# Performance work log

Hardware: AMD Instinct MI355X
Metric: run time of the kernel (lower is better)

Reference implementation:

```python
import jax, jax.numpy as jnp
import numpy as np
from jax import lax

B, C_IN, L = 16, 4, 300000
KERNEL, ANCHOR_N = 11, 16
LEAK = 1e-4
EPS = 1e-12  # torch F.normalize eps


def setup_inputs() -> dict:
    key = jax.random.key(0)
    k1, k2, k3 = jax.random.split(key, 3)
    data = jax.random.normal(k1, (B, C_IN, L), dtype=jnp.float32)
    # Conv1d weights, PyTorch default init scale ~ U(-s, s), s = 1/sqrt(fan_in)
    s = 1.0 / np.sqrt(C_IN * KERNEL)
    W = jax.random.uniform(k2, (ANCHOR_N, C_IN, KERNEL), dtype=jnp.float32, minval=-s, maxval=s)
    b = jax.random.uniform(k3, (ANCHOR_N,), dtype=jnp.float32, minval=-s, maxval=s)
    return {"data": data, "W": W, "b": b, "anchor_index": 3}


def reference(data, W, b, anchor_index):
    # Conv1d(4 -> anchor_n, valid padding) + LeakyReLU(0.0001)
    y = lax.conv_general_dilated(
        data, W, window_strides=(1,), padding="VALID",
        dimension_numbers=("NCH", "OIH", "NCH"))
    y = y + b[None, :, None]                      # [B, anchor_n, Lc]
    y = jnp.where(y > 0, y, LEAK * y)
    # select anchor channel, add leading dim -> [1, B, Lc]
    ch = y[:, anchor_index, :][None]
    # F.normalize(dim=2, p=1)
    denom = jnp.maximum(jnp.sum(jnp.abs(ch), axis=2, keepdims=True), EPS)
    channel = ch / denom
    # softmax over sequence dim (gamma = 1)
    dist = jax.nn.softmax(channel, axis=2)
    # weighted moments of position distribution (single pass each)
    Lc = dist.shape[2]
    x = jnp.arange(Lc, dtype=dist.dtype)          # positions
    mean = jnp.sum(dist * x, axis=2, keepdims=True)    # [1,B,1]
    x_diff = x - mean                                   # [1,B,Lc]
    var = jnp.sum(dist * x_diff * x_diff, axis=2, keepdims=True)
    z = x_diff / jnp.sqrt(var)
    z3 = z * z * z
    skews = jnp.mean(z3, axis=2)                  # [1,B]
    kts = jnp.mean(z3 * z, axis=2) - 3.0          # [1,B]
    return (skews, kts, channel)
```

## Files before the change

### kernel.cpp

```cpp
#include <hip/hip_runtime.h>
#include <math.h>

#define BATCH 16
#define CIN 4
#define LEN 300000
#define KW 11
#define LC (LEN - KW + 1)
#define LCP 300000
#define LEAK 1e-4f
#define EPS_N 1e-12f

#define NB 64
#define CHUNK 4688
#define TILE 1024
#define ROW 1040


__global__ __launch_bounds__(256) void conv_stats(
    const float* __restrict__ data, const float* __restrict__ W,
    const float* __restrict__ bias, const int* __restrict__ aidx,
    double* __restrict__ absP, float* __restrict__ maxP,
    float* __restrict__ ch)
{
    const int b = blockIdx.y, j = blockIdx.x, tid = threadIdx.x;
    __shared__ float sd[CIN][ROW];

    const int a = aidx[0];
    float w[CIN * KW];
#pragma unroll
    for (int k = 0; k < CIN * KW; ++k) w[k] = W[a * CIN * KW + k];
    const float sb = bias[a];

    const float* dbase = data + (size_t)b * (CIN * (size_t)LEN);
    float* chrow = ch + (size_t)b * LCP;

    const int cstart = j * CHUNK;
    const int cend   = min(cstart + CHUNK, LC);

    float aabs = 0.0f;
    float amax = -INFINITY;

    for (int l0 = cstart; l0 < cend; l0 += TILE) {
        const int n    = min(TILE, cend - l0);
        const int need = n + 14;
        const int nv   = (need + 3) >> 2;
        __syncthreads();
#pragma unroll
        for (int c = 0; c < CIN; ++c) {
            const float* src = dbase + (size_t)c * LEN + l0;
            for (int i = tid; i < nv; i += 256) {
                const int off = i << 2;
                float4 v;
                if (l0 + off + 3 < LEN) {
                    v = *(const float4*)(src + off);
                } else {
                    v.x = (l0 + off     < LEN) ? src[off]     : 0.0f;
                    v.y = (l0 + off + 1 < LEN) ? src[off + 1] : 0.0f;
                    v.z = (l0 + off + 2 < LEN) ? src[off + 2] : 0.0f;
                    v.w = (l0 + off + 3 < LEN) ? src[off + 3] : 0.0f;
                }
                *(float4*)(&sd[c][off]) = v;
            }
        }
        __syncthreads();

        const int n4 = n >> 2;
        for (int q = tid; q < n4; q += 256) {
            const int o = q << 2;
            float acc0 = sb, acc1 = sb, acc2 = sb, acc3 = sb;
#pragma unroll
            for (int c = 0; c < CIN; ++c) {
                float x[16];
                const float4 v0 = *(const float4*)(&sd[c][o]);
                const float4 v1 = *(const float4*)(&sd[c][o + 4]);
                const float4 v2 = *(const float4*)(&sd[c][o + 8]);
                const float4 v3 = *(const float4*)(&sd[c][o + 12]);
                x[0] = v0.x;  x[1] = v0.y;  x[2]  = v0.z;  x[3]  = v0.w;
                x[4] = v1.x;  x[5] = v1.y;  x[6]  = v1.z;  x[7]  = v1.w;
                x[8] = v2.x;  x[9] = v2.y;  x[10] = v2.z;  x[11] = v2.w;
                x[12] = v3.x; x[13] = v3.y; x[14] = v3.z;  x[15] = v3.w;
#pragma unroll
                for (int k = 0; k < KW; ++k) {
                    const float wv = w[c * KW + k];
                    acc0 = fmaf(x[k],     wv, acc0);
                    acc1 = fmaf(x[k + 1], wv, acc1);
                    acc2 = fmaf(x[k + 2], wv, acc2);
                    acc3 = fmaf(x[k + 3], wv, acc3);
                }
            }
            float4 y;
            y.x = acc0 > 0.0f ? acc0 : LEAK * acc0;
            y.y = acc1 > 0.0f ? acc1 : LEAK * acc1;
            y.z = acc2 > 0.0f ? acc2 : LEAK * acc2;
            y.w = acc3 > 0.0f ? acc3 : LEAK * acc3;
            *(float4*)(chrow + l0 + o) = y;
            aabs += (fabsf(y.x) + fabsf(y.y)) + (fabsf(y.z) + fabsf(y.w));
            amax = fmaxf(amax, fmaxf(fmaxf(y.x, y.y), fmaxf(y.z, y.w)));
        }
        for (int q = (n4 << 2) + tid; q < n; q += 256) {
            float acc = sb;
#pragma unroll
            for (int c = 0; c < CIN; ++c)
#pragma unroll
                for (int k = 0; k < KW; ++k)
                    acc = fmaf(sd[c][q + k], w[c * KW + k], acc);
            float y = acc > 0.0f ? acc : LEAK * acc;
            chrow[l0 + q] = y;
            aabs += fabsf(y);
            amax = fmaxf(amax, y);
        }
    }

#pragma unroll
    for (int off = 32; off; off >>= 1) {
        aabs += __shfl_down(aabs, off);
        amax  = fmaxf(amax, __shfl_down(amax, off));
    }
    __shared__ float ra[4], rm[4];
    const int wv = tid >> 6;
    if ((tid & 63) == 0) { ra[wv] = aabs; rm[wv] = amax; }
    __syncthreads();
    if (tid == 0) {
        absP[b * NB + j] = (double)((ra[0] + ra[1]) + (ra[2] + ra[3]));
        maxP[b * NB + j] = fmaxf(fmaxf(rm[0], rm[1]), fmaxf(rm[2], rm[3]));
    }
}

__global__ void reduce1(const double* __restrict__ absP,
                        const float* __restrict__ maxP,
                        float* __restrict__ stats)
{
    const int b = blockIdx.x, t = threadIdx.x;
    double s = (t < NB) ? absP[b * NB + t] : 0.0;
    float  m = (t < NB) ? maxP[b * NB + t] : -INFINITY;
#pragma unroll
    for (int off = 32; off; off >>= 1) {
        s += __shfl_down(s, off);
        m  = fmaxf(m, __shfl_down(m, off));
    }
    if (t == 0) {
        stats[b * 2]     = fmaxf((float)s, EPS_N);
        stats[b * 2 + 1] = m;
    }
}

__global__ __launch_bounds__(256) void softmax_pass(
    const float* __restrict__ ch, const float* __restrict__ stats,
    float* __restrict__ chan_out, double* __restrict__ sP)
{
    const int b = blockIdx.y, j = blockIdx.x, tid = threadIdx.x;
    const float denom = stats[b * 2];
    const float inv   = 1.0f / denom;
    const float mx    = stats[b * 2 + 1] * inv;

    const float* src = ch + (size_t)b * LCP;
    float* dst = chan_out + (size_t)b * LC;

    const int cstart = j * CHUNK;
    const int cend   = min(cstart + CHUNK, LC);

    double te = 0.0, t1 = 0.0, t2 = 0.0;

    const int nfull = (cend - cstart) >> 2;
    for (int q = tid; q < nfull; q += 256) {
        const int l = cstart + (q << 2);
        const float4 v = *(const float4*)(src + l);
        float cc[4] = { v.x * inv, v.y * inv, v.z * inv, v.w * inv };
        float2 p0 = { cc[0], cc[1] };
        float2 p1 = { cc[2], cc[3] };
        *(float2*)(dst + l)     = p0;
        *(float2*)(dst + l + 2) = p1;
#pragma unroll
        for (int u = 0; u < 4; ++u) {
            const float e = expf(cc[u] - mx);
            const double xd = (double)(l + u);
            te += (double)e;
            t1 += (double)e * xd;
            t2 += (double)e * xd * xd;
        }
    }
    for (int l = cstart + (nfull << 2) + tid; l < cend; l += 256) {
        const float c = src[l] * inv;
        dst[l] = c;
        const float e = expf(c - mx);
        const double xd = (double)l;
        te += (double)e;
        t1 += (double)e * xd;
        t2 += (double)e * xd * xd;
    }

#pragma unroll
    for (int off = 32; off; off >>= 1) {
        te += __shfl_down(te, off);
        t1 += __shfl_down(t1, off);
        t2 += __shfl_down(t2, off);
    }
    __shared__ double we[4], w1[4], w2[4];
    const int wv = tid >> 6;
    if ((tid & 63) == 0) { we[wv] = te; w1[wv] = t1; w2[wv] = t2; }
    __syncthreads();
    if (tid == 0) {
        double* p = sP + (size_t)(b * NB + j) * 3;
        p[0] = (we[0] + we[1]) + (we[2] + we[3]);
        p[1] = (w1[0] + w1[1]) + (w1[2] + w1[3]);
        p[2] = (w2[0] + w2[1]) + (w2[2] + w2[3]);
    }
}

__global__ void finalize(const double* __restrict__ sP, float* __restrict__ out)
{
    const int b = blockIdx.x, t = threadIdx.x;
    double te = 0.0, t1 = 0.0, t2 = 0.0;
    if (t < NB) {
        const double* p = sP + (size_t)(b * NB + t) * 3;
        te = p[0]; t1 = p[1]; t2 = p[2];
    }
#pragma unroll
    for (int off = 32; off; off >>= 1) {
        te += __shfl_down(te, off);
        t1 += __shfl_down(t1, off);
        t2 += __shfl_down(t2, off);
    }
    if (t == 0) {
        const double E    = te;
        const double mean = t1 / E;
        const double var  = t2 / E - mean * mean;

        const double n   = (double)LC;
        const double nm1 = n - 1.0;
        const double S1p = 0.5 * n * nm1;
        const double S2p = nm1 * n * (2.0 * n - 1.0) / 6.0;
        const double S3p = S1p * S1p;
        const double S4p = S2p * (3.0 * n * n - 3.0 * n - 1.0) / 5.0;

        const double mu  = mean;
        const double mu2 = mu * mu;
        const double P3 = S3p - 3.0 * mu * S2p + 3.0 * mu2 * S1p - n * mu * mu2;
        const double P4 = S4p - 4.0 * mu * S3p + 6.0 * mu2 * S2p
                          - 4.0 * mu * mu2 * S1p + n * mu2 * mu2;

        const double sv   = sqrt(var);
        const double skew = P3 / (n * sv * sv * sv);
        const double kurt = P4 / (n * var * var) - 3.0;

        out[b]         = (float)skew;
        out[BATCH + b] = (float)kurt;
    }
}

extern "C" void kernel_launch(void* const* d_in, const int* in_sizes, int n_in,
                              void* d_out, int out_size, void* d_ws, size_t ws_size,
                              hipStream_t stream) {
    const float* data = (const float*)d_in[0];
    const float* W    = (const float*)d_in[1];
    const float* bias = (const float*)d_in[2];
    const int*   aidx = (const int*)d_in[3];
    float* out = (float*)d_out;

    char* ws = (char*)d_ws;
    double* absP  = (double*)(ws + 0);
    float*  maxP  = (float*) (ws + 8192);
    float*  stats = (float*) (ws + 12288);
    double* sP    = (double*)(ws + 12416);
    float*  ch    = (float*) (ws + 65536);

    dim3 grid(NB, BATCH);
    conv_stats<<<grid, dim3(256), 0, stream>>>(data, W, bias, aidx, absP, maxP, ch);
    reduce1<<<dim3(BATCH), dim3(64), 0, stream>>>(absP, maxP, stats);
    softmax_pass<<<grid, dim3(256), 0, stream>>>(ch, stats, out + 2 * BATCH, sP);
    finalize<<<dim3(BATCH), dim3(64), 0, stream>>>(sP, out);
}
```

Before: 148.5 us.

## Fold reduction kernels into main passes via last-block ticket; register-tiled conv

The conv pass drops its shared-memory staging. Each thread now loads a 28-float window per channel straight from global memory and computes 16 outputs in registers, and the grid grows to about 74 blocks per batch. The separate reduce1 and finalize kernels are removed. The last block to finish, chosen by an atomic ticket counter reset with a memset, now does those reductions. The softmax pass now accumulates moments in float per thread and adds the position offset in double, and it alternates float4 and float2 stores by batch parity. This cuts kernel launches and shared-memory traffic, at the cost of overlapping unaligned global loads and float-precision partial moments.

```diff
diff --git a/kernel.cpp b/kernel.cpp
--- a/kernel.cpp
+++ b/kernel.cpp
@@ -10,22 +10,22 @@
 #define LEAK 1e-4f
 #define EPS_N 1e-12f
 
-#define NB 64
-#define CHUNK 4688
-#define TILE 1024
-#define ROW 1040
+#define TPB 256
+#define EPT 16
+#define BPB (TPB * EPT)
+#define NBX ((LC + BPB - 1) / BPB)
+#define NBLK (NBX * BATCH)
 
 
 __global__ __launch_bounds__(256) void conv_stats(
     const float* __restrict__ data, const float* __restrict__ W,
     const float* __restrict__ bias, const int* __restrict__ aidx,
-    double* __restrict__ absP, float* __restrict__ maxP,
-    float* __restrict__ ch)
+    float* __restrict__ ch, double* __restrict__ absP, float* __restrict__ maxP,
+    float* __restrict__ stats, unsigned* __restrict__ ticket)
 {
     const int b = blockIdx.y, j = blockIdx.x, tid = threadIdx.x;
-    __shared__ float sd[CIN][ROW];
-
-    const int a = aidx[0];
+    const int a = __builtin_amdgcn_readfirstlane(aidx[0]);
+
     float w[CIN * KW];
 #pragma unroll
     for (int k = 0; k < CIN * KW; ++k) w[k] = W[a * CIN * KW + k];
@@ -33,160 +33,150 @@
 
     const float* dbase = data + (size_t)b * (CIN * (size_t)LEN);
     float* chrow = ch + (size_t)b * LCP;
-
-    const int cstart = j * CHUNK;
-    const int cend   = min(cstart + CHUNK, LC);
-
-    float aabs = 0.0f;
-    float amax = -INFINITY;
-
-    for (int l0 = cstart; l0 < cend; l0 += TILE) {
-        const int n    = min(TILE, cend - l0);
-        const int need = n + 14;
-        const int nv   = (need + 3) >> 2;
-        __syncthreads();
+    const int o = j * BPB + tid * EPT;
+
+    float aabs = 0.0f, amax = -INFINITY;
+
+    if (o + EPT <= LC) {
+        float acc[EPT];
+#pragma unroll
+        for (int u = 0; u < EPT; ++u) acc[u] = sb;
 #pragma unroll
         for (int c = 0; c < CIN; ++c) {
-            const float* src = dbase + (size_t)c * LEN + l0;
-            for (int i = tid; i < nv; i += 256) {
-                const int off = i << 2;
-                float4 v;
-                if (l0 + off + 3 < LEN) {
-                    v = *(const float4*)(src + off);
-                } else {
-                    v.x = (l0 + off     < LEN) ? src[off]     : 0.0f;
-                    v.y = (l0 + off + 1 < LEN) ? src[off + 1] : 0.0f;
-                    v.z = (l0 + off + 2 < LEN) ? src[off + 2] : 0.0f;
-                    v.w = (l0 + off + 3 < LEN) ? src[off + 3] : 0.0f;
-                }
-                *(float4*)(&sd[c][off]) = v;
-            }
-        }
-        __syncthreads();
-
-        const int n4 = n >> 2;
-        for (int q = tid; q < n4; q += 256) {
-            const int o = q << 2;
-            float acc0 = sb, acc1 = sb, acc2 = sb, acc3 = sb;
-#pragma unroll
-            for (int c = 0; c < CIN; ++c) {
-                float x[16];
-                const float4 v0 = *(const float4*)(&sd[c][o]);
-                const float4 v1 = *(const float4*)(&sd[c][o + 4]);
-                const float4 v2 = *(const float4*)(&sd[c][o + 8]);
-                const float4 v3 = *(const float4*)(&sd[c][o + 12]);
-                x[0] = v0.x;  x[1] = v0.y;  x[2]  = v0.z;  x[3]  = v0.w;
-                x[4] = v1.x;  x[5] = v1.y;  x[6]  = v1.z;  x[7]  = v1.w;
-                x[8] = v2.x;  x[9] = v2.y;  x[10] = v2.z;  x[11] = v2.w;
-                x[12] = v3.x; x[13] = v3.y; x[14] = v3.z;  x[15] = v3.w;
-#pragma unroll
-                for (int k = 0; k < KW; ++k) {
-                    const float wv = w[c * KW + k];
-                    acc0 = fmaf(x[k],     wv, acc0);
-                    acc1 = fmaf(x[k + 1], wv, acc1);
-                    acc2 = fmaf(x[k + 2], wv, acc2);
-                    acc3 = fmaf(x[k + 3], wv, acc3);
-                }
-            }
-            float4 y;
-            y.x = acc0 > 0.0f ? acc0 : LEAK * acc0;
-            y.y = acc1 > 0.0f ? acc1 : LEAK * acc1;
-            y.z = acc2 > 0.0f ? acc2 : LEAK * acc2;
-            y.w = acc3 > 0.0f ? acc3 : LEAK * acc3;
-            *(float4*)(chrow + l0 + o) = y;
-            aabs += (fabsf(y.x) + fabsf(y.y)) + (fabsf(y.z) + fabsf(y.w));
-            amax = fmaxf(amax, fmaxf(fmaxf(y.x, y.y), fmaxf(y.z, y.w)));
-        }
-        for (int q = (n4 << 2) + tid; q < n; q += 256) {
-            float acc = sb;
-#pragma unroll
-            for (int c = 0; c < CIN; ++c)
+            const float* src = dbase + (size_t)c * LEN + o;
+            float x[28];
+#pragma unroll
+            for (int i = 0; i < 7; ++i) {
+                const float4 v = *(const float4*)(src + 4 * i);
+                x[4 * i] = v.x; x[4 * i + 1] = v.y;
+                x[4 * i + 2] = v.z; x[4 * i + 3] = v.w;
+            }
+#pragma unroll
+            for (int u = 0; u < EPT; ++u)
 #pragma unroll
                 for (int k = 0; k < KW; ++k)
-                    acc = fmaf(sd[c][q + k], w[c * KW + k], acc);
-            float y = acc > 0.0f ? acc : LEAK * acc;
-            chrow[l0 + q] = y;
+                    acc[u] = fmaf(x[u + k], w[c * KW + k], acc[u]);
+        }
+#pragma unroll
+        for (int u = 0; u < EPT; ++u) {
+            const float y = acc[u] > 0.0f ? acc[u] : LEAK * acc[u];
+            acc[u] = y;
             aabs += fabsf(y);
             amax = fmaxf(amax, y);
         }
+#pragma unroll
+        for (int i = 0; i < 4; ++i)
+            *(float4*)(chrow + o + 4 * i) =
+                make_float4(acc[4 * i], acc[4 * i + 1], acc[4 * i + 2], acc[4 * i + 3]);
+    } else {
+        for (int l = o; l < LC; ++l) {
+            float accv = sb;
+#pragma unroll
+            for (int c = 0; c < CIN; ++c)
+#pragma unroll
+                for (int k = 0; k < KW; ++k)
+                    accv = fmaf(dbase[(size_t)c * LEN + l + k], w[c * KW + k], accv);
+            const float y = accv > 0.0f ? accv : LEAK * accv;
+            chrow[l] = y;
+            aabs += fabsf(y);
+            amax = fmaxf(amax, y);
+        }
     }
 
 #pragma unroll
     for (int off = 32; off; off >>= 1) {
         aabs += __shfl_down(aabs, off);
-        amax  = fmaxf(amax, __shfl_down(amax, off));
+        amax = fmaxf(amax, __shfl_down(amax, off));
     }
     __shared__ float ra[4], rm[4];
+    __shared__ bool last;
     const int wv = tid >> 6;
     if ((tid & 63) == 0) { ra[wv] = aabs; rm[wv] = amax; }
     __syncthreads();
     if (tid == 0) {
-        absP[b * NB + j] = (double)((ra[0] + ra[1]) + (ra[2] + ra[3]));
-        maxP[b * NB + j] = fmaxf(fmaxf(rm[0], rm[1]), fmaxf(rm[2], rm[3]));
-    }
-}
-
-__global__ void reduce1(const double* __restrict__ absP,
-                        const float* __restrict__ maxP,
-                        float* __restrict__ stats)
-{
-    const int b = blockIdx.x, t = threadIdx.x;
-    double s = (t < NB) ? absP[b * NB + t] : 0.0;
-    float  m = (t < NB) ? maxP[b * NB + t] : -INFINITY;
-#pragma unroll
-    for (int off = 32; off; off >>= 1) {
-        s += __shfl_down(s, off);
-        m  = fmaxf(m, __shfl_down(m, off));
-    }
-    if (t == 0) {
-        stats[b * 2]     = fmaxf((float)s, EPS_N);
-        stats[b * 2 + 1] = m;
+        absP[b * NBX + j] = (double)((ra[0] + ra[1]) + (ra[2] + ra[3]));
+        maxP[b * NBX + j] = fmaxf(fmaxf(rm[0], rm[1]), fmaxf(rm[2], rm[3]));
+        __threadfence();
+        last = (atomicAdd(ticket, 1u) == NBLK - 1);
+    }
+    __syncthreads();
+    if (last) {
+        __threadfence();
+        const int wave = tid >> 6, lane = tid & 63;
+        for (int bb = wave; bb < BATCH; bb += 4) {
+            double s = 0.0; float m = -INFINITY;
+            for (int i = lane; i < NBX; i += 64) {
+                s += absP[bb * NBX + i];
+                m = fmaxf(m, maxP[bb * NBX + i]);
+            }
+#pragma unroll
+            for (int off = 32; off; off >>= 1) {
+                s += __shfl_down(s, off);
+                m = fmaxf(m, __shfl_down(m, off));
+            }
+            if (lane == 0) {
+                stats[2 * bb]     = fmaxf((float)s, EPS_N);
+                stats[2 * bb + 1] = m;
+            }
+        }
     }
 }
 
 __global__ __launch_bounds__(256) void softmax_pass(
     const float* __restrict__ ch, const float* __restrict__ stats,
-    float* __restrict__ chan_out, double* __restrict__ sP)
+    float* __restrict__ chan_out, double* __restrict__ sP,
+    float* __restrict__ out, unsigned* __restrict__ ticket)
 {
     const int b = blockIdx.y, j = blockIdx.x, tid = threadIdx.x;
-    const float denom = stats[b * 2];
-    const float inv   = 1.0f / denom;
-    const float mx    = stats[b * 2 + 1] * inv;
+    const float inv = 1.0f / stats[2 * b];
+    const float mx  = stats[2 * b + 1] * inv;
 
     const float* src = ch + (size_t)b * LCP;
     float* dst = chan_out + (size_t)b * LC;
-
-    const int cstart = j * CHUNK;
-    const int cend   = min(cstart + CHUNK, LC);
+    const int o = j * BPB + tid * EPT;
 
     double te = 0.0, t1 = 0.0, t2 = 0.0;
 
-    const int nfull = (cend - cstart) >> 2;
-    for (int q = tid; q < nfull; q += 256) {
-        const int l = cstart + (q << 2);
-        const float4 v = *(const float4*)(src + l);
-        float cc[4] = { v.x * inv, v.y * inv, v.z * inv, v.w * inv };
-        float2 p0 = { cc[0], cc[1] };
-        float2 p1 = { cc[2], cc[3] };
-        *(float2*)(dst + l)     = p0;
-        *(float2*)(dst + l + 2) = p1;
-#pragma unroll
-        for (int u = 0; u < 4; ++u) {
+    if (o + EPT <= LC) {
+        float cc[EPT];
+#pragma unroll
+        for (int i = 0; i < 4; ++i) {
+            const float4 v = *(const float4*)(src + o + 4 * i);
+            cc[4 * i] = v.x * inv; cc[4 * i + 1] = v.y * inv;
+            cc[4 * i + 2] = v.z * inv; cc[4 * i + 3] = v.w * inv;
+        }
+        if ((b & 1) == 0) {
+#pragma unroll
+            for (int i = 0; i < 4; ++i)
+                *(float4*)(dst + o + 4 * i) =
+                    make_float4(cc[4 * i], cc[4 * i + 1], cc[4 * i + 2], cc[4 * i + 3]);
+        } else {
+#pragma unroll
+            for (int i = 0; i < 8; ++i)
+                *(float2*)(dst + o + 2 * i) = make_float2(cc[2 * i], cc[2 * i + 1]);
+        }
+        float se = 0.0f, su = 0.0f, suu = 0.0f;
+#pragma unroll
+        for (int u = 0; u < EPT; ++u) {
             const float e = expf(cc[u] - mx);
-            const double xd = (double)(l + u);
+            se += e;
+            su += e * (float)u;
+            suu += e * (float)(u * u);
+        }
+        const double od = (double)o;
+        te = (double)se;
+        t1 = od * (double)se + (double)su;
+        t2 = od * od * (double)se + 2.0 * od * (double)su + (double)suu;
+    } else {
+        for (int l = o; l < LC; ++l) {
+            const float c = src[l] * inv;
+            dst[l] = c;
+            const float e = expf(c - mx);
+            const double xd = (double)l;
             te += (double)e;
             t1 += (double)e * xd;
             t2 += (double)e * xd * xd;
         }
-    }
-    for (int l = cstart + (nfull << 2) + tid; l < cend; l += 256) {
-        const float c = src[l] * inv;
-        dst[l] = c;
-        const float e = expf(c - mx);
-        const double xd = (double)l;
-        te += (double)e;
-        t1 += (double)e * xd;
-        t2 += (double)e * xd * xd;
     }
 
 #pragma unroll
@@ -196,55 +186,56 @@
         t2 += __shfl_down(t2, off);
     }
     __shared__ double we[4], w1[4], w2[4];
+    __shared__ bool last;
     const int wv = tid >> 6;
     if ((tid & 63) == 0) { we[wv] = te; w1[wv] = t1; w2[wv] = t2; }
     __syncthreads();
     if (tid == 0) {
-        double* p = sP + (size_t)(b * NB + j) * 3;
+        double* p = sP + (size_t)(b * NBX + j) * 3;
         p[0] = (we[0] + we[1]) + (we[2] + we[3]);
         p[1] = (w1[0] + w1[1]) + (w1[2] + w1[3]);
         p[2] = (w2[0] + w2[1]) + (w2[2] + w2[3]);
-    }
-}
-
-__global__ void finalize(const double* __restrict__ sP, float* __restrict__ out)
-{
-    const int b = blockIdx.x, t = threadIdx.x;
-    double te = 0.0, t1 = 0.0, t2 = 0.0;
-    if (t < NB) {
-        const double* p = sP + (size_t)(b * NB + t) * 3;
-        te = p[0]; t1 = p[1]; t2 = p[2];
-    }
-#pragma unroll
-    for (int off = 32; off; off >>= 1) {
-        te += __shfl_down(te, off);
-        t1 += __shfl_down(t1, off);
-        t2 += __shfl_down(t2, off);
-    }
-    if (t == 0) {
-        const double E    = te;
-        const double mean = t1 / E;
-        const double var  = t2 / E - mean * mean;
-
-        const double n   = (double)LC;
-        const double nm1 = n - 1.0;
-        const double S1p = 0.5 * n * nm1;
-        const double S2p = nm1 * n * (2.0 * n - 1.0) / 6.0;
-        const double S3p = S1p * S1p;
-        const double S4p = S2p * (3.0 * n * n - 3.0 * n - 1.0) / 5.0;
-
-        const double mu  = mean;
-        const double mu2 = mu * mu;
-        const double P3 = S3p - 3.0 * mu * S2p + 3.0 * mu2 * S1p - n * mu * mu2;
-        const double P4 = S4p - 4.0 * mu * S3p + 6.0 * mu2 * S2p
-                          - 4.0 * mu * mu2 * S1p + n * mu2 * mu2;
-
-        const double sv   = sqrt(var);
-        const double skew = P3 / (n * sv * sv * sv);
-        const double kurt = P4 / (n * var * var) - 3.0;
-
-        out[b]         = (float)skew;
-        out[BATCH + b] = (float)kurt;
+        __threadfence();
+        last = (atomicAdd(ticket, 1u) == NBLK - 1);
+    }
+    __syncthreads();
+    if (last) {
+        __threadfence();
+        const int wave = tid >> 6, lane = tid & 63;
+        for (int bb = wave; bb < BATCH; bb += 4) {
+            double e = 0.0, m1 = 0.0, m2 = 0.0;
+            for (int i = lane; i < NBX; i += 64) {
+                const double* p = sP + (size_t)(bb * NBX + i) * 3;
+                e += p[0]; m1 += p[1]; m2 += p[2];
+            }
+#pragma unroll
+            for (int off = 32; off; off >>= 1) {
+                e  += __shfl_down(e, off);
+                m1 += __shfl_down(m1, off);
+                m2 += __shfl_down(m2, off);
+            }
+            if (lane == 0) {
+                const double mean = m1 / e;
+                const double var  = m2 / e - mean * mean;
+
+                const double n   = (double)LC;
+                const double nm1 = n - 1.0;
+                const double S1p = 0.5 * n * nm1;
+                const double S2p = nm1 * n * (2.0 * n - 1.0) / 6.0;
+                const double S3p = S1p * S1p;
+                const double S4p = S2p * (3.0 * n * n - 3.0 * n - 1.0) / 5.0;
+
+                const double mu  = mean;
+                const double mu2 = mu * mu;
+                const double P3 = S3p - 3.0 * mu * S2p + 3.0 * mu2 * S1p - n * mu * mu2;
+                const double P4 = S4p - 4.0 * mu * S3p + 6.0 * mu2 * S2p
+                                  - 4.0 * mu * mu2 * S1p + n * mu2 * mu2;
+
+                const double sv = sqrt(var);
+                out[bb]         = (float)(P3 / (n * sv * sv * sv));
+                out[BATCH + bb] = (float)(P4 / (n * var * var) - 3.0);
+            }
+        }
     }
 }
 
@@ -258,15 +249,18 @@
     float* out = (float*)d_out;
 
     char* ws = (char*)d_ws;
-    double* absP  = (double*)(ws + 0);
-    float*  maxP  = (float*) (ws + 8192);
-    float*  stats = (float*) (ws + 12288);
-    double* sP    = (double*)(ws + 12416);
-    float*  ch    = (float*) (ws + 65536);
-
-    dim3 grid(NB, BATCH);
-    conv_stats<<<grid, dim3(256), 0, stream>>>(data, W, bias, aidx, absP, maxP, ch);
-    reduce1<<<dim3(BATCH), dim3(64), 0, stream>>>(absP, maxP, stats);
-    softmax_pass<<<grid, dim3(256), 0, stream>>>(ch, stats, out + 2 * BATCH, sP);
-    finalize<<<dim3(BATCH), dim3(64), 0, stream>>>(sP, out);
+    unsigned* ticket = (unsigned*)(ws + 0);
+    double*   absP   = (double*)  (ws + 1024);
+    float*    maxP   = (float*)   (ws + 10752);
+    float*    stats  = (float*)   (ws + 15616);
+    double*   sP     = (double*)  (ws + 16384);
+    float*    ch     = (float*)   (ws + 65536);
+
+    hipMemsetAsync(ticket, 0, 16, stream);
+
+    dim3 grid(NBX, BATCH);
+    conv_stats<<<grid, dim3(TPB), 0, stream>>>(data, W, bias, aidx, ch,
+                                               absP, maxP, stats, ticket);
+    softmax_pass<<<grid, dim3(TPB), 0, stream>>>(ch, stats, out + 2 * BATCH, sP,
+                                                 out, ticket + 1);
 }
```

Result: slower. 296.2 us (+99.4%).
